# Kernel optimization log

Measured on AMD Instinct MI355X. Metric: run time of the kernel, lower is better.

The kernel has to match this reference:

```python
import jax, jax.numpy as jnp
import numpy as np

MAX_SEQ_LEN = 2048
ADJ_SCALE = 0.1


def setup_inputs() -> dict:
    key = jax.random.key(0)
    k1, k2, k3 = jax.random.split(key, 3)
    B, L, H, D = 8, 2048, 16, 64
    x = jax.random.normal(k1, (B, L, H, D), dtype=jnp.float32)
    W = jax.random.normal(k2, (D, D), dtype=jnp.float32) * (1.0 / np.sqrt(D))
    b = jax.random.normal(k3, (D,), dtype=jnp.float32) * 0.02
    gate = jnp.ones((1,), dtype=jnp.float32) * 0.5  # betweenness_gate init
    return {"x": x, "W": W, "b": b, "gate": gate}


def reference(x, W, b, gate):
    B, L, H, D = x.shape
    # --- RoPE frequency table (precompute_freqs_cis) ---
    base_freqs = 1.0 / (10000.0 ** (jnp.arange(0, D, 2, dtype=jnp.float32) / D))  # (D/2,)
    t = jnp.arange(L, dtype=jnp.float32)
    freqs = t[:, None] * base_freqs[None, :]          # (L, D/2)
    fcos, fsin = jnp.cos(freqs), jnp.sin(freqs)

    # --- betweenness: only consecutive-pair distances are ever used ---
    content = jnp.einsum('blhd,ed->blhe', x, W) + b    # nn.Linear(dim, dim)
    d1 = jnp.linalg.norm(content[:, 1:] - content[:, :-1], axis=-1)   # (B, L-1, H)  d(i, i+1)
    d2 = jnp.linalg.norm(content[:, 2:] - content[:, :-2], axis=-1)   # (B, L-2, H)  d(i, i+2)
    direct = d2
    path = d1[:, :-1] + d1[:, 1:]
    score = jax.nn.relu(1.0 - (path - direct) / jnp.maximum(direct, 1e-6))  # (B, L-2, H)
    betweenness = jnp.zeros((B, L, H), x.dtype).at[:, 1:L - 1].set(score / (L - 2))

    # --- betweenness-adjusted interpolated RoPE (vectorized over positions) ---
    adjust = gate[0] * (betweenness - 0.5) * ADJ_SCALE               # (B, L, H)
    pos = jnp.arange(L, dtype=jnp.float32)[None, :, None]
    adj_pos = jnp.clip(pos + adjust, 0.0, MAX_SEQ_LEN - 1)
    lo = jnp.floor(adj_pos).astype(jnp.int32)
    hi = jnp.ceil(adj_pos).astype(jnp.int32)
    frac = (adj_pos - lo)[..., None]                                 # (B, L, H, 1)
    cos_i = (1.0 - frac) * fcos[lo] + frac * fcos[hi]                # (B, L, H, D/2)
    sin_i = (1.0 - frac) * fsin[lo] + frac * fsin[hi]

    x_even = x[..., 0::2]
    x_odd = x[..., 1::2]
    out_even = x_even * cos_i - x_odd * sin_i
    out_odd = x_odd * cos_i + x_even * sin_i
    out = jnp.stack([out_even, out_odd], axis=-1).reshape(B, L, H, D)  # re-interleave
    return out
```

## Files before the change

kernel.cpp:

```cpp
#include <hip/hip_runtime.h>

#define L_SEQ 2048
#define HEADS 16
#define DIM   64
#define TILE  32
#define XROWS 34
#define XPITCH 68
#define DROWS 48

typedef __attribute__((ext_vector_type(8))) short bf16x8;
typedef __attribute__((ext_vector_type(4))) float f32x4;

__device__ unsigned short g_mbf[DIM * DIM];

static __device__ __forceinline__ unsigned short f2bf_rtne(float f) {
    unsigned int u = __builtin_bit_cast(unsigned int, f);
    u += 0x7fffu + ((u >> 16) & 1u);
    return (unsigned short)(u >> 16);
}
static __device__ __forceinline__ unsigned int pk2(float a, float b) {
    return __builtin_amdgcn_perm(__builtin_bit_cast(unsigned int, b),
                                 __builtin_bit_cast(unsigned int, a), 0x07060302u);
}
static __device__ __forceinline__ float bfhi(unsigned int u) {
    return __builtin_bit_cast(float, u << 16);
}
static __device__ __forceinline__ float bflo(unsigned int u) {
    return __builtin_bit_cast(float, u & 0xffff0000u);
}

#define SWZ(row, col) ((row) * 64 + ((col) ^ (((row) & 7) * 8)))

__global__ void prep_m_kernel(const float* __restrict__ W) {
    const int i = blockIdx.x, j = threadIdx.x;
    float acc = 0.f;
    #pragma unroll 8
    for (int e = 0; e < DIM; ++e)
        acc = fmaf(W[e * DIM + i], W[e * DIM + j], acc);
    g_mbf[i * DIM + j] = f2bf_rtne(acc);
}

__global__ __launch_bounds__(256) void betweenness_rope_kernel(
    const float* __restrict__ x, const float* __restrict__ gate,
    float* __restrict__ out)
{
    __shared__ float xs[XROWS * XPITCH];
    __shared__ unsigned short dl[DROWS * 64];
    __shared__ float psq[4][DROWS];
    __shared__ float ppr[4][DROWS];
    __shared__ float2 fl[TILE];

    const int tid  = threadIdx.x;
    const int lane = tid & 63;
    const int wv   = tid >> 6;
    const int la   = lane & 15, lg = lane >> 4;
    const int l0   = blockIdx.x * TILE;
    const int h    = blockIdx.y;
    const int b    = blockIdx.z;
    const int bh_off = (b * L_SEQ * HEADS + h) * DIM;

    for (int s = tid; s < 392; s += 256) {
        if (s < 272) {
            int r = s >> 3, c0 = (s & 7) * 8;
            int g = max(0, min(L_SEQ - 1, l0 - 1 + r));
            const float* px = x + bh_off + g * (HEADS * DIM) + c0;
            float4 x0 = *(const float4*)px;
            float4 x1 = *(const float4*)(px + 4);
            *(float4*)&xs[r * XPITCH + c0]     = x0;
            *(float4*)&xs[r * XPITCH + c0 + 4] = x1;
            if (r < 33) {
                int g1 = min(L_SEQ - 1, l0 + r);
                const float* py = x + bh_off + g1 * (HEADS * DIM) + c0;
                float4 y0 = *(const float4*)py;
                float4 y1 = *(const float4*)(py + 4);
                uint4 o;
                o.x = pk2(y0.x - x0.x, y0.y - x0.y);
                o.y = pk2(y0.z - x0.z, y0.w - x0.w);
                o.z = pk2(y1.x - x1.x, y1.y - x1.y);
                o.w = pk2(y1.z - x1.z, y1.w - x1.w);
                *(uint4*)&dl[SWZ(r, c0)] = o;
            }
        } else {
            int z = s - 272;
            int r = 33 + (z >> 3), c0 = (z & 7) * 8;
            uint4 o = {0u, 0u, 0u, 0u};
            *(uint4*)&dl[SWZ(r, c0)] = o;
        }
    }
    __syncthreads();

    {
        const int abase = (16 * wv + la) * 64 + lg * 8;
        bf16x8 ma0 = *(const bf16x8*)&g_mbf[abase];
        bf16x8 ma1 = *(const bf16x8*)&g_mbf[abase + 32];
        const int c = 16 * wv + 4 * lg;
        #pragma unroll
        for (int rt = 0; rt < 3; ++rt) {
            int br = 16 * rt + la;
            bf16x8 bb0 = *(const bf16x8*)&dl[SWZ(br, lg * 8)];
            bf16x8 bb1 = *(const bf16x8*)&dl[SWZ(br, lg * 8 + 32)];
            f32x4 d = {0.f, 0.f, 0.f, 0.f};
            d = __builtin_amdgcn_mfma_f32_16x16x32_bf16(ma0, bb0, d, 0, 0, 0);
            d = __builtin_amdgcn_mfma_f32_16x16x32_bf16(ma1, bb1, d, 0, 0, 0);
            uint2 duv = *(const uint2*)&dl[SWZ(br, c)];
            int br1 = min(br + 1, DROWS - 1);
            uint2 dvv = *(const uint2*)&dl[SWZ(br1, c)];
            float n1p = d[0] * bfhi(duv.x);
            n1p = fmaf(d[1], bflo(duv.x), n1p);
            n1p = fmaf(d[2], bfhi(duv.y), n1p);
            n1p = fmaf(d[3], bflo(duv.y), n1p);
            float g1p = d[0] * bfhi(dvv.x);
            g1p = fmaf(d[1], bflo(dvv.x), g1p);
            g1p = fmaf(d[2], bfhi(dvv.y), g1p);
            g1p = fmaf(d[3], bflo(dvv.y), g1p);
            n1p += __shfl_xor(n1p, 16, 64);
            g1p += __shfl_xor(g1p, 16, 64);
            n1p += __shfl_xor(n1p, 32, 64);
            g1p += __shfl_xor(g1p, 32, 64);
            if (lg == 0) { psq[wv][br] = n1p; ppr[wv][br] = g1p; }
        }
    }
    __syncthreads();

    if (tid < TILE) {
        const float gate0 = gate[0];
        int r = tid, l = l0 + r;
        float n1a = psq[0][r]     + psq[1][r]     + psq[2][r]     + psq[3][r];
        float n1b = psq[0][r + 1] + psq[1][r + 1] + psq[2][r + 1] + psq[3][r + 1];
        float gg  = ppr[0][r]     + ppr[1][r]     + ppr[2][r]     + ppr[3][r];
        float d1a = sqrtf(n1a), d1b = sqrtf(n1b);
        float dd  = sqrtf(fmaxf(n1a + n1b + 2.f * gg, 0.f));
        float sc  = fmaxf(1.f - ((d1a + d1b) - dd) / fmaxf(dd, 1e-6f), 0.f);
        float bet = (l >= 1 && l <= L_SEQ - 2) ? sc * (1.f / (L_SEQ - 2)) : 0.f;
        float adjust = gate0 * (bet - 0.5f) * 0.1f;
        float ap  = fminf(fmaxf((float)l + adjust, 0.f), (float)(L_SEQ - 1));
        float flo = floorf(ap);
        fl[r] = make_float2(flo, ap - flo);
    }
    __syncthreads();

    {
        const int j = lane & 31, half = lane >> 5;
        const float fjr = __builtin_exp2f(-0.4152410118609203f * (float)j)
                        * 0.15915494309189535f;
        const float cf = __builtin_amdgcn_cosf(fjr);
        const float sf = __builtin_amdgcn_sinf(fjr);
        const float cfm1 = cf - 1.0f;
        const int r0w = wv * 2 + half;
        const float* xbase = &xs[(r0w + 1) * XPITCH + 2 * j];
        float* obase = out + bh_off + (l0 + r0w) * (HEADS * DIM) + 2 * j;
        #pragma unroll
        for (int it = 0; it < 4; ++it) {
            int r = it * 8 + r0w;
            float2 ff = fl[r];
            float t0 = ff.x * fjr;
            float rv = t0 - floorf(t0);
            float c_lo = __builtin_amdgcn_cosf(rv);
            float s_lo = __builtin_amdgcn_sinf(rv);
            float u = fmaf(ff.y, cfm1, 1.0f);
            float v = ff.y * sf;
            float ci = fmaf(-s_lo, v, c_lo * u);
            float si = fmaf(c_lo, v, s_lo * u);
            float2 xv = *(const float2*)(xbase + it * 8 * XPITCH);
            float2 o;
            o.x = xv.x * ci - xv.y * si;
            o.y = fmaf(xv.y, ci, xv.x * si);
            *(float2*)(obase + it * 8 * (HEADS * DIM)) = o;
        }
    }
}

extern "C" void kernel_launch(void* const* d_in, const int* in_sizes, int n_in,
                              void* d_out, int out_size, void* d_ws, size_t ws_size,
                              hipStream_t stream) {
    const float* x    = (const float*)d_in[0];
    const float* W    = (const float*)d_in[1];
    const float* gate = (const float*)d_in[3];
    float* out = (float*)d_out;

    const int B = in_sizes[0] / (L_SEQ * HEADS * DIM);

    prep_m_kernel<<<DIM, DIM, 0, stream>>>(W);

    dim3 grid(L_SEQ / TILE, HEADS, B);
    betweenness_rope_kernel<<<grid, 256, 0, stream>>>(x, gate, out);
}
```

Baseline: 42.76 us.

## Process four tiles per block with register-prefetched x rows

Each block now walks four consecutive 32-row tiles and prefetches the next tile's x rows into registers while the current tile's MFMA and RoPE stages run. Consecutive differences are built from shared memory instead of a second global load, which removes the duplicated read of neighbouring rows. The aim is to hide global-load latency and cut redundant traffic. In exchange the grid is four times smaller, there are more barriers per block, and register pressure is higher under the added occupancy hint.

```diff
diff --git a/kernel.cpp b/kernel.cpp
--- a/kernel.cpp
+++ b/kernel.cpp
@@ -4,6 +4,7 @@
 #define HEADS 16
 #define DIM   64
 #define TILE  32
+#define NTILES 4
 #define XROWS 34
 #define XPITCH 68
 #define DROWS 48
@@ -40,7 +41,7 @@
     g_mbf[i * DIM + j] = f2bf_rtne(acc);
 }
 
-__global__ __launch_bounds__(256) void betweenness_rope_kernel(
+__global__ __launch_bounds__(256, 8) void betweenness_rope_kernel(
     const float* __restrict__ x, const float* __restrict__ gate,
     float* __restrict__ out)
 {
@@ -54,118 +55,161 @@
     const int lane = tid & 63;
     const int wv   = tid >> 6;
     const int la   = lane & 15, lg = lane >> 4;
-    const int l0   = blockIdx.x * TILE;
     const int h    = blockIdx.y;
     const int b    = blockIdx.z;
     const int bh_off = (b * L_SEQ * HEADS + h) * DIM;
-
-    for (int s = tid; s < 392; s += 256) {
-        if (s < 272) {
-            int r = s >> 3, c0 = (s & 7) * 8;
-            int g = max(0, min(L_SEQ - 1, l0 - 1 + r));
-            const float* px = x + bh_off + g * (HEADS * DIM) + c0;
-            float4 x0 = *(const float4*)px;
-            float4 x1 = *(const float4*)(px + 4);
-            *(float4*)&xs[r * XPITCH + c0]     = x0;
-            *(float4*)&xs[r * XPITCH + c0 + 4] = x1;
-            if (r < 33) {
-                int g1 = min(L_SEQ - 1, l0 + r);
-                const float* py = x + bh_off + g1 * (HEADS * DIM) + c0;
-                float4 y0 = *(const float4*)py;
-                float4 y1 = *(const float4*)(py + 4);
-                uint4 o;
-                o.x = pk2(y0.x - x0.x, y0.y - x0.y);
-                o.y = pk2(y0.z - x0.z, y0.w - x0.w);
-                o.z = pk2(y1.x - x1.x, y1.y - x1.y);
-                o.w = pk2(y1.z - x1.z, y1.w - x1.w);
-                *(uint4*)&dl[SWZ(r, c0)] = o;
+    const int l0q  = blockIdx.x * (TILE * NTILES);
+    const float gate0 = gate[0];
+
+    const int r_a = tid >> 3, c_a = (tid & 7) * 8;
+    const bool hasB = (tid < 16);
+    const int r_b = 32 + (tid >> 3);
+
+    float4 pfa0, pfa1, pfb0 = {0,0,0,0}, pfb1 = {0,0,0,0};
+    auto prefetch = [&](int tt) {
+        int l0t = l0q + tt * TILE;
+        int ga = max(0, min(L_SEQ - 1, l0t - 1 + r_a));
+        const float* pa = x + bh_off + ga * (HEADS * DIM) + c_a;
+        pfa0 = *(const float4*)pa;
+        pfa1 = *(const float4*)(pa + 4);
+        if (hasB) {
+            int gb = max(0, min(L_SEQ - 1, l0t - 1 + r_b));
+            const float* pb = x + bh_off + gb * (HEADS * DIM) + c_a;
+            pfb0 = *(const float4*)pb;
+            pfb1 = *(const float4*)(pb + 4);
+        }
+    };
+    auto write_xs = [&]() {
+        *(float4*)&xs[r_a * XPITCH + c_a]     = pfa0;
+        *(float4*)&xs[r_a * XPITCH + c_a + 4] = pfa1;
+        if (hasB) {
+            *(float4*)&xs[r_b * XPITCH + c_a]     = pfb0;
+            *(float4*)&xs[r_b * XPITCH + c_a + 4] = pfb1;
+        }
+    };
+
+    const int j = lane & 31, half = lane >> 5;
+    const int r0w = wv * 2 + half;
+    const float fjr = __builtin_exp2f(-0.4152410118609203f * (float)j)
+                    * 0.15915494309189535f;
+    const float cf = __builtin_amdgcn_cosf(fjr);
+    const float sf = __builtin_amdgcn_sinf(fjr);
+    const float cfm1 = cf - 1.0f;
+
+    if (tid < 120) {
+        int r = 33 + (tid >> 3), c0 = (tid & 7) * 8;
+        uint4 z = {0u, 0u, 0u, 0u};
+        *(uint4*)&dl[SWZ(r, c0)] = z;
+    }
+
+    prefetch(0);
+    write_xs();
+    prefetch(1);
+    __syncthreads();
+
+    for (int it = 0; it < NTILES; ++it) {
+        const int l0 = l0q + it * TILE;
+
+        {
+            float4 a0 = *(float4*)&xs[r_a * XPITCH + c_a];
+            float4 a1 = *(float4*)&xs[r_a * XPITCH + c_a + 4];
+            float4 b0 = *(float4*)&xs[(r_a + 1) * XPITCH + c_a];
+            float4 b1 = *(float4*)&xs[(r_a + 1) * XPITCH + c_a + 4];
+            uint4 o;
+            o.x = pk2(b0.x - a0.x, b0.y - a0.y);
+            o.y = pk2(b0.z - a0.z, b0.w - a0.w);
+            o.z = pk2(b1.x - a1.x, b1.y - a1.y);
+            o.w = pk2(b1.z - a1.z, b1.w - a1.w);
+            *(uint4*)&dl[SWZ(r_a, c_a)] = o;
+            if (tid < 8) {
+                float4 c0v = *(float4*)&xs[32 * XPITCH + c_a];
+                float4 c1v = *(float4*)&xs[32 * XPITCH + c_a + 4];
+                float4 d0v = *(float4*)&xs[33 * XPITCH + c_a];
+                float4 d1v = *(float4*)&xs[33 * XPITCH + c_a + 4];
+                uint4 o2;
+                o2.x = pk2(d0v.x - c0v.x, d0v.y - c0v.y);
+                o2.y = pk2(d0v.z - c0v.z, d0v.w - c0v.w);
+                o2.z = pk2(d1v.x - c1v.x, d1v.y - c1v.y);
+                o2.w = pk2(d1v.z - c1v.z, d1v.w - c1v.w);
+                *(uint4*)&dl[SWZ(32, c_a)] = o2;
             }
-        } else {
-            int z = s - 272;
-            int r = 33 + (z >> 3), c0 = (z & 7) * 8;
-            uint4 o = {0u, 0u, 0u, 0u};
-            *(uint4*)&dl[SWZ(r, c0)] = o;
-        }
-    }
-    __syncthreads();
-
-    {
-        const int abase = (16 * wv + la) * 64 + lg * 8;
-        bf16x8 ma0 = *(const bf16x8*)&g_mbf[abase];
-        bf16x8 ma1 = *(const bf16x8*)&g_mbf[abase + 32];
-        const int c = 16 * wv + 4 * lg;
+        }
+        float2 xv[4];
         #pragma unroll
-        for (int rt = 0; rt < 3; ++rt) {
-            int br = 16 * rt + la;
-            bf16x8 bb0 = *(const bf16x8*)&dl[SWZ(br, lg * 8)];
-            bf16x8 bb1 = *(const bf16x8*)&dl[SWZ(br, lg * 8 + 32)];
-            f32x4 d = {0.f, 0.f, 0.f, 0.f};
-            d = __builtin_amdgcn_mfma_f32_16x16x32_bf16(ma0, bb0, d, 0, 0, 0);
-            d = __builtin_amdgcn_mfma_f32_16x16x32_bf16(ma1, bb1, d, 0, 0, 0);
-            uint2 duv = *(const uint2*)&dl[SWZ(br, c)];
-            int br1 = min(br + 1, DROWS - 1);
-            uint2 dvv = *(const uint2*)&dl[SWZ(br1, c)];
-            float n1p = d[0] * bfhi(duv.x);
-            n1p = fmaf(d[1], bflo(duv.x), n1p);
-            n1p = fmaf(d[2], bfhi(duv.y), n1p);
-            n1p = fmaf(d[3], bflo(duv.y), n1p);
-            float g1p = d[0] * bfhi(dvv.x);
-            g1p = fmaf(d[1], bflo(dvv.x), g1p);
-            g1p = fmaf(d[2], bfhi(dvv.y), g1p);
-            g1p = fmaf(d[3], bflo(dvv.y), g1p);
-            n1p += __shfl_xor(n1p, 16, 64);
-            g1p += __shfl_xor(g1p, 16, 64);
-            n1p += __shfl_xor(n1p, 32, 64);
-            g1p += __shfl_xor(g1p, 32, 64);
-            if (lg == 0) { psq[wv][br] = n1p; ppr[wv][br] = g1p; }
-        }
-    }
-    __syncthreads();
-
-    if (tid < TILE) {
-        const float gate0 = gate[0];
-        int r = tid, l = l0 + r;
-        float n1a = psq[0][r]     + psq[1][r]     + psq[2][r]     + psq[3][r];
-        float n1b = psq[0][r + 1] + psq[1][r + 1] + psq[2][r + 1] + psq[3][r + 1];
-        float gg  = ppr[0][r]     + ppr[1][r]     + ppr[2][r]     + ppr[3][r];
-        float d1a = sqrtf(n1a), d1b = sqrtf(n1b);
-        float dd  = sqrtf(fmaxf(n1a + n1b + 2.f * gg, 0.f));
-        float sc  = fmaxf(1.f - ((d1a + d1b) - dd) / fmaxf(dd, 1e-6f), 0.f);
-        float bet = (l >= 1 && l <= L_SEQ - 2) ? sc * (1.f / (L_SEQ - 2)) : 0.f;
-        float adjust = gate0 * (bet - 0.5f) * 0.1f;
-        float ap  = fminf(fmaxf((float)l + adjust, 0.f), (float)(L_SEQ - 1));
-        float flo = floorf(ap);
-        fl[r] = make_float2(flo, ap - flo);
-    }
-    __syncthreads();
-
-    {
-        const int j = lane & 31, half = lane >> 5;
-        const float fjr = __builtin_exp2f(-0.4152410118609203f * (float)j)
-                        * 0.15915494309189535f;
-        const float cf = __builtin_amdgcn_cosf(fjr);
-        const float sf = __builtin_amdgcn_sinf(fjr);
-        const float cfm1 = cf - 1.0f;
-        const int r0w = wv * 2 + half;
-        const float* xbase = &xs[(r0w + 1) * XPITCH + 2 * j];
-        float* obase = out + bh_off + (l0 + r0w) * (HEADS * DIM) + 2 * j;
-        #pragma unroll
-        for (int it = 0; it < 4; ++it) {
-            int r = it * 8 + r0w;
-            float2 ff = fl[r];
-            float t0 = ff.x * fjr;
-            float rv = t0 - floorf(t0);
-            float c_lo = __builtin_amdgcn_cosf(rv);
-            float s_lo = __builtin_amdgcn_sinf(rv);
-            float u = fmaf(ff.y, cfm1, 1.0f);
-            float v = ff.y * sf;
-            float ci = fmaf(-s_lo, v, c_lo * u);
-            float si = fmaf(c_lo, v, s_lo * u);
-            float2 xv = *(const float2*)(xbase + it * 8 * XPITCH);
-            float2 o;
-            o.x = xv.x * ci - xv.y * si;
-            o.y = fmaf(xv.y, ci, xv.x * si);
-            *(float2*)(obase + it * 8 * (HEADS * DIM)) = o;
+        for (int k = 0; k < 4; ++k)
+            xv[k] = *(const float2*)&xs[(r0w + 1 + 8 * k) * XPITCH + 2 * j];
+        __syncthreads();
+
+        {
+            const int abase = (16 * wv + la) * 64 + lg * 8;
+            bf16x8 ma0 = *(const bf16x8*)&g_mbf[abase];
+            bf16x8 ma1 = *(const bf16x8*)&g_mbf[abase + 32];
+            const int c = 16 * wv + 4 * lg;
+            #pragma unroll
+            for (int rt = 0; rt < 3; ++rt) {
+                int br = 16 * rt + la;
+                bf16x8 bb0 = *(const bf16x8*)&dl[SWZ(br, lg * 8)];
+                bf16x8 bb1 = *(const bf16x8*)&dl[SWZ(br, lg * 8 + 32)];
+                f32x4 d = {0.f, 0.f, 0.f, 0.f};
+                d = __builtin_amdgcn_mfma_f32_16x16x32_bf16(ma0, bb0, d, 0, 0, 0);
+                d = __builtin_amdgcn_mfma_f32_16x16x32_bf16(ma1, bb1, d, 0, 0, 0);
+                uint2 duv = *(const uint2*)&dl[SWZ(br, c)];
+                int br1 = min(br + 1, DROWS - 1);
+                uint2 dvv = *(const uint2*)&dl[SWZ(br1, c)];
+                float n1p = d[0] * bfhi(duv.x);
+                n1p = fmaf(d[1], bflo(duv.x), n1p);
+                n1p = fmaf(d[2], bfhi(duv.y), n1p);
+                n1p = fmaf(d[3], bflo(duv.y), n1p);
+                float g1p = d[0] * bfhi(dvv.x);
+                g1p = fmaf(d[1], bflo(dvv.x), g1p);
+                g1p = fmaf(d[2], bfhi(dvv.y), g1p);
+                g1p = fmaf(d[3], bflo(dvv.y), g1p);
+                n1p += __shfl_xor(n1p, 16, 64);
+                g1p += __shfl_xor(g1p, 16, 64);
+                n1p += __shfl_xor(n1p, 32, 64);
+                g1p += __shfl_xor(g1p, 32, 64);
+                if (lg == 0) { psq[wv][br] = n1p; ppr[wv][br] = g1p; }
+            }
+        }
+        if (it + 1 < NTILES) write_xs();
+        __syncthreads();
+
+        if (tid < TILE) {
+            int r = tid, l = l0 + r;
+            float n1a = psq[0][r]     + psq[1][r]     + psq[2][r]     + psq[3][r];
+            float n1b = psq[0][r + 1] + psq[1][r + 1] + psq[2][r + 1] + psq[3][r + 1];
+            float gg  = ppr[0][r]     + ppr[1][r]     + ppr[2][r]     + ppr[3][r];
+            float d1a = sqrtf(n1a), d1b = sqrtf(n1b);
+            float dd  = sqrtf(fmaxf(n1a + n1b + 2.f * gg, 0.f));
+            float sc  = fmaxf(1.f - ((d1a + d1b) - dd) / fmaxf(dd, 1e-6f), 0.f);
+            float bet = (l >= 1 && l <= L_SEQ - 2) ? sc * (1.f / (L_SEQ - 2)) : 0.f;
+            float adjust = gate0 * (bet - 0.5f) * 0.1f;
+            float ap  = fminf(fmaxf((float)l + adjust, 0.f), (float)(L_SEQ - 1));
+            float flo = floorf(ap);
+            fl[r] = make_float2(flo, ap - flo);
+        }
+        if (it < NTILES - 2) prefetch(it + 2);
+        __syncthreads();
+
+        {
+            float* obase = out + bh_off + (l0 + r0w) * (HEADS * DIM) + 2 * j;
+            #pragma unroll
+            for (int k = 0; k < 4; ++k) {
+                int r = k * 8 + r0w;
+                float2 ff = fl[r];
+                float t0 = ff.x * fjr;
+                float rv = t0 - floorf(t0);
+                float c_lo = __builtin_amdgcn_cosf(rv);
+                float s_lo = __builtin_amdgcn_sinf(rv);
+                float u = fmaf(ff.y, cfm1, 1.0f);
+                float v = ff.y * sf;
+                float ci = fmaf(-s_lo, v, c_lo * u);
+                float si = fmaf(c_lo, v, s_lo * u);
+                float2 o;
+                o.x = xv[k].x * ci - xv[k].y * si;
+                o.y = fmaf(xv[k].y, ci, xv[k].x * si);
+                *(float2*)(obase + k * 8 * (HEADS * DIM)) = o;
+            }
         }
     }
 }
@@ -182,6 +226,6 @@
 
     prep_m_kernel<<<DIM, DIM, 0, stream>>>(W);
 
-    dim3 grid(L_SEQ / TILE, HEADS, B);
+    dim3 grid(L_SEQ / (TILE * NTILES), HEADS, B);
     betweenness_rope_kernel<<<grid, 256, 0, stream>>>(x, gate, out);
 }
```

Result: slower. 46.60 us (+9.0%).
